# Kernel tuning notes

Measured on AMD Instinct MI355X. Metric: run time of the kernel, lower is better.

The kernel has to match this reference:

```python
import jax, jax.numpy as jnp
import numpy as np

NDIM = 128
GDIM = 128
NUM_LAYERS = 2
B = 8192
IDX = 16          # nodes per graph
EPG = 32          # edges per graph
N = B * IDX       # total nodes = 131072
E = B * EPG       # total edges = 262144


def setup_inputs() -> dict:
    key = jax.random.key(0)
    ks = jax.random.split(key, 24)
    h = jax.random.normal(ks[0], (B, IDX, NDIM), dtype=jnp.float32)
    # edges constrained within each graph (flattened node indexing)
    gid = jnp.repeat(jnp.arange(B, dtype=jnp.int64), EPG)
    src = gid * IDX + jax.random.randint(ks[1], (E,), 0, IDX).astype(jnp.int64)
    dst = gid * IDX + jax.random.randint(ks[2], (E,), 0, IDX).astype(jnp.int64)
    edge_index = jnp.stack([src, dst], axis=0)
    s = 0.05
    inp = {
        'h': h,
        'edge_index': edge_index,
        'msg_W': jax.random.normal(ks[3], (NUM_LAYERS, 2 * NDIM, 2 * NDIM), jnp.float32) * s,
        'msg_b': jax.random.normal(ks[4], (NUM_LAYERS, 2 * NDIM), jnp.float32) * s,
        'msgr_W': jax.random.normal(ks[5], (NUM_LAYERS, 2 * NDIM, 2 * NDIM), jnp.float32) * s,
        'msgr_b': jax.random.normal(ks[6], (NUM_LAYERS, 2 * NDIM), jnp.float32) * s,
        'gru_Wih': jax.random.normal(ks[7], (NUM_LAYERS, 3 * NDIM, 2 * NDIM), jnp.float32) * s,
        'gru_Whh': jax.random.normal(ks[8], (NUM_LAYERS, 3 * NDIM, NDIM), jnp.float32) * s,
        'gru_bih': jax.random.normal(ks[9], (NUM_LAYERS, 3 * NDIM), jnp.float32) * s,
        'gru_bhh': jax.random.normal(ks[10], (NUM_LAYERS, 3 * NDIM), jnp.float32) * s,
        'fm_W': jax.random.normal(ks[11], (GDIM, NDIM), jnp.float32) * s,
        'fm_b': jax.random.normal(ks[12], (GDIM,), jnp.float32) * s,
        'gm_W': jax.random.normal(ks[13], (1, NDIM), jnp.float32) * s,
        'gm_b': jax.random.normal(ks[14], (1,), jnp.float32) * s,
        'fmi_W': jax.random.normal(ks[15], (GDIM, NDIM), jnp.float32) * s,
        'fmi_b': jax.random.normal(ks[16], (GDIM,), jnp.float32) * s,
        'gmi_W': jax.random.normal(ks[17], (1, NDIM), jnp.float32) * s,
        'gmi_b': jax.random.normal(ks[18], (1,), jnp.float32) * s,
    }
    return inp


def _gnn_forward(h, edge_index, msg_W, msg_b, msgr_W, msgr_b,
                 gru_Wih, gru_Whh, gru_bih, gru_bhh):
    # h: [N, ndim]; edge_index: [2, E] -> doubled with reversed edges -> [2, 2E]
    ei = jnp.concatenate([edge_index, edge_index[::-1]], axis=1)
    src, dst = ei[0], ei[1]
    e = edge_index.shape[1]
    n_nodes = h.shape[0]
    for l in range(NUM_LAYERS):
        # (eval mode: dropout p=0.0 is a no-op)
        h_j = h[src]                       # [2E, ndim]
        h_i = h[dst]                       # [2E, ndim]
        m = jnp.concatenate([h_j, h_i], axis=1)   # [2E, 2*ndim]
        m_fwd, m_rev = m[:e], m[e:]
        a = jnp.concatenate([
            m_fwd @ msg_W[l].T + msg_b[l],
            m_rev @ msgr_W[l].T + msgr_b[l],
        ], axis=0)                          # [2E, 2*ndim]
        aggr = jax.ops.segment_sum(a, dst, num_segments=n_nodes)  # [N, 2*ndim]
        # GRUCell(aggr, h): gate order r, z, n (torch convention)
        gi = aggr @ gru_Wih[l].T + gru_bih[l]   # [N, 3*ndim]
        gh = h @ gru_Whh[l].T + gru_bhh[l]      # [N, 3*ndim]
        gi_r, gi_z, gi_n = jnp.split(gi, 3, axis=1)
        gh_r, gh_z, gh_n = jnp.split(gh, 3, axis=1)
        r = jax.nn.sigmoid(gi_r + gh_r)
        z = jax.nn.sigmoid(gi_z + gh_z)
        n = jnp.tanh(gi_n + r * gh_n)
        h = n + z * (h - n)                 # (1-z)*n + z*h
    return h


def _graph_aggr(h, idx, f_W, f_b, g_W, g_b):
    # gated sum aggregation
    h_vG = h @ f_W.T + f_b                      # [N, gdim]
    g_vG = jax.nn.sigmoid(h @ g_W.T + g_b)      # [N, 1]
    out = (h_vG * g_vG).reshape(-1, idx, f_W.shape[0])
    return out.sum(axis=1)                      # [B, gdim]


def reference(h, edge_index, msg_W, msg_b, msgr_W, msgr_b,
              gru_Wih, gru_Whh, gru_bih, gru_bhh,
              fm_W, fm_b, gm_W, gm_b, fmi_W, fmi_b, gmi_W, gmi_b):
    idx = h.shape[1]
    hf = h.reshape(-1, NDIM)
    hf = _gnn_forward(hf, edge_index, msg_W, msg_b, msgr_W, msgr_b,
                      gru_Wih, gru_Whh, gru_bih, gru_bhh)
    h_G = _graph_aggr(hf, idx, fm_W, fm_b, gm_W, gm_b)
    h_G_init = _graph_aggr(hf, idx, fmi_W, fmi_b, gmi_W, gmi_b)
    return (hf.reshape(-1, idx, NDIM), h_G, h_G_init)
```

## Files before the change

### kernel.cpp

```cpp
#include <hip/hip_runtime.h>
#include <math.h>
#include <stdint.h>

#define NDIM 128
#define B_GRAPHS 8192
#define IDX 16
#define EPG 32
#define NN (B_GRAPHS*IDX)
#define NE (B_GRAPHS*EPG)

typedef short bf16x8 __attribute__((ext_vector_type(8)));
typedef float f32x4  __attribute__((ext_vector_type(4)));
typedef unsigned short u16x4 __attribute__((ext_vector_type(4)));

__device__ inline unsigned short f2bf(float x) {
    union { float f; unsigned u; } v; v.f = x;
    unsigned r = v.u + 0x7fff + ((v.u >> 16) & 1);
    return (unsigned short)(r >> 16);
}
__device__ inline float bf2f(unsigned short b) {
    union { unsigned u; float f; } v; v.u = ((unsigned)b) << 16;
    return v.f;
}
__device__ inline float sigm(float x) { return 1.f/(1.f + __expf(-x)); }
__device__ inline float tanh_f(float x) {
    float ax = fabsf(x);
    float t  = __expf(-2.f*ax);
    float r  = (1.f - t)/(1.f + t);
    return copysignf(r, x);
}

#define GLOAD_LDS16(g, l) \
    __builtin_amdgcn_global_load_lds( \
        (const __attribute__((address_space(1))) unsigned int*)(g), \
        (__attribute__((address_space(3))) unsigned int*)(l), 16, 0, 0)

__global__ __launch_bounds__(256) void compose_kernel(
    const float* __restrict__ msg_W, const float* __restrict__ msgr_W,
    const float* __restrict__ Wih,   const float* __restrict__ Whh,
    const float* __restrict__ msg_b, const float* __restrict__ msgr_b,
    unsigned short* __restrict__ WB, float* __restrict__ c34)
{
    int idx = blockIdx.x*256 + threadIdx.x;
    const int TWB = 2*512*640;
    if (idx < TWB) {
        int l = idx / (512*640); int rem = idx - l*(512*640);
        int c = rem / 640; int k = rem - c*640;
        float val;
        if (k < 512) {
            if (c < 384) {
                const float* wih = Wih + l*384*256 + c*256;
                const float* M; int sc;
                if (k < 128)      { M = msg_W  + l*256*256; sc = k;       }
                else if (k < 256) { M = msgr_W + l*256*256; sc = k - 128; }
                else if (k < 384) { M = msg_W  + l*256*256; sc = k - 128; }
                else              { M = msgr_W + l*256*256; sc = k - 256; }
                float acc = 0.f;
                for (int q = 0; q < 256; q++) acc = fmaf(wih[q], M[q*256 + sc], acc);
                val = acc;
            } else val = 0.f;
        } else {
            int kk = k - 512;
            if (c < 256)      val = Whh[l*384*128 + c*128 + kk];
            else if (c < 384) val = 0.f;
            else              val = Whh[l*384*128 + (c-128)*128 + kk];
        }
        WB[idx] = f2bf(val);
    } else if (idx < TWB + 2*2*384) {
        int i2 = idx - TWB;
        int l = i2 / 768; int rem = i2 - l*768;
        int which = rem / 384; int r = rem - which*384;
        const float* wih = Wih + l*384*256 + r*256;
        const float* bb  = (which ? msgr_b : msg_b) + l*256;
        float acc = 0.f;
        for (int q = 0; q < 256; q++) acc = fmaf(wih[q], bb[q], acc);
        c34[l*768 + which*384 + r] = acc;
    }
}

__global__ __launch_bounds__(128) void init_kernel(
    const float* __restrict__ hin, const int* __restrict__ ei,
    unsigned short* __restrict__ A, float* __restrict__ indeg,
    float* __restrict__ outdeg, unsigned char* __restrict__ pack)
{
    int g = blockIdx.x, t = threadIdx.x;
    __shared__ float hb[16][128];
    __shared__ float sin_[16][128];
    __shared__ float sout_[16][128];
    __shared__ int sl[32], dl[32];
    __shared__ int cin[16], cout[16];
    __shared__ int flag64;
    int base = g*IDX;
    for (int r = 0; r < 16; r++) hb[r][t] = hin[(size_t)(base+r)*128 + t];
    for (int r = 0; r < 16; r++) { sin_[r][t] = 0.f; sout_[r][t] = 0.f; }
    if (t < 16) { cin[t] = 0; cout[t] = 0; }
    if (t == 0) {
        int orv = 0;
        for (int i = 1; i < 64; i += 2) orv |= ei[i];
        flag64 = (orv == 0);
    }
    __syncthreads();
    if (t < 32) {
        int e = g*EPG + t;
        int sv, dv;
        if (flag64) { sv = ei[2*e]; dv = ei[2*(NE + e)]; }
        else        { sv = ei[e];   dv = ei[NE + e];     }
        sl[t] = sv - base; dl[t] = dv - base;
        atomicAdd(&cout[sl[t]], 1); atomicAdd(&cin[dl[t]], 1);
        pack[g*32 + t] = (unsigned char)((sl[t] & 15) | ((dl[t] & 15) << 4));
    }
    __syncthreads();
    for (int e = 0; e < 32; e++) {
        sin_[dl[e]][t]  += hb[sl[e]][t];
        sout_[sl[e]][t] += hb[dl[e]][t];
    }
    for (int r = 0; r < 16; r++) {
        size_t v = base + r;
        float di = (float)cin[r], dof = (float)cout[r];
        A[v*640 + t]        = f2bf(sin_[r][t]);
        A[v*640 + 128 + t]  = f2bf(sout_[r][t]);
        A[v*640 + 256 + t]  = f2bf(di  * hb[r][t]);
        A[v*640 + 384 + t]  = f2bf(dof * hb[r][t]);
        A[v*640 + 512 + t]  = f2bf(hb[r][t]);
    }
    if (t < 16) { indeg[base+t] = (float)cin[t]; outdeg[base+t] = (float)cout[t]; }
}

struct LoopBufs { unsigned short As[3][4096]; unsigned short Bs[3][16384]; };
union UnionRegion {
    LoopBufs lp;
    unsigned short Gs[512*128];
    float sio[2][128][128];
};
struct SmemT { UnionRegion u; unsigned short hnewB[128][128]; };

__device__ __forceinline__ void stage_tile(
    const unsigned short* __restrict__ A, const unsigned short* __restrict__ WB,
    int n0, int kc, unsigned short* As, unsigned short* Bs, int tid)
{
    {
        int row = tid >> 2, s = tid & 3;
        int slot = s ^ ((row >> 2) & 3);
        GLOAD_LDS16(A + (size_t)(n0 + row)*640 + kc + slot*8, As + row*32 + s*8);
    }
#pragma unroll
    for (int i = 0; i < 4; i++) {
        int u = i*512 + tid; int col = u >> 2, s = u & 3;
        int slot = s ^ ((col >> 2) & 3);
        GLOAD_LDS16(WB + (size_t)col*640 + kc + slot*8, Bs + col*32 + s*8);
    }
}

template <bool FINAL>
__global__ __launch_bounds__(512, 2) void fused_kernel(
    unsigned short* __restrict__ A,
    const unsigned short* __restrict__ WB,
    const float* __restrict__ indeg, const float* __restrict__ outdeg,
    const unsigned char* __restrict__ pack,
    const float* __restrict__ c34l,
    const float* __restrict__ bihl, const float* __restrict__ bhhl,
    float* __restrict__ hf)
{
    __shared__ SmemT sm;
    const int n0  = blockIdx.x * 128;
    const int tid = threadIdx.x;
    const int lane = tid & 63;
    const int wc  = tid >> 6;
    const int l15 = lane & 15, l4 = lane >> 4;

    int ks_lo = 0, ks_hi = 20;
    if (wc == 4 || wc == 5) ks_hi = 16;
    if (wc >= 6)            ks_lo = 16;

    f32x4 acc[8][4] = {};

    stage_tile(A, WB, n0, 0,  sm.u.lp.As[0], sm.u.lp.Bs[0], tid);
    stage_tile(A, WB, n0, 32, sm.u.lp.As[1], sm.u.lp.Bs[1], tid);
    asm volatile("s_waitcnt vmcnt(5)\n\ts_barrier" ::: "memory");

    for (int ks = 0; ks < 20; ks++) {
        int buf = ks % 3;
        if (ks + 2 < 20) {
            int nb = (ks + 2) % 3;
            stage_tile(A, WB, n0, (ks+2)*32, sm.u.lp.As[nb], sm.u.lp.Bs[nb], tid);
        }
        if (ks >= ks_lo && ks < ks_hi) {
            bf16x8 af[8], bfv[4];
            int slot = l4 ^ ((l15 >> 2) & 3);
            const unsigned short* Asb = sm.u.lp.As[buf];
            const unsigned short* Bsb = sm.u.lp.Bs[buf];
#pragma unroll
            for (int mi = 0; mi < 8; mi++)
                af[mi] = *(const bf16x8*)(Asb + (mi*16 + l15)*32 + slot*8);
#pragma unroll
            for (int ni = 0; ni < 4; ni++)
                bfv[ni] = *(const bf16x8*)(Bsb + (wc*64 + ni*16 + l15)*32 + slot*8);
#pragma unroll
            for (int mi = 0; mi < 8; mi++)
#pragma unroll
                for (int ni = 0; ni < 4; ni++)
                    acc[mi][ni] = __builtin_amdgcn_mfma_f32_16x16x32_bf16(
                        af[mi], bfv[ni], acc[mi][ni], 0, 0, 0);
        }
        if (ks + 2 < 20)
            asm volatile("s_waitcnt vmcnt(5)\n\ts_barrier" ::: "memory");
        else
            asm volatile("s_waitcnt vmcnt(0)\n\ts_barrier" ::: "memory");
    }

#pragma unroll
    for (int mi = 0; mi < 8; mi++) {
        int row0  = mi*16 + l4*4;
        int slotA = row0 >> 3;
        int half  = (row0 >> 2) & 1;
#pragma unroll
        for (int ni = 0; ni < 4; ni++) {
            int col = wc*64 + ni*16 + l15;
            int slot2 = slotA ^ (col & 15);
            u16x4 w;
            w[0] = f2bf(acc[mi][ni][0]); w[1] = f2bf(acc[mi][ni][1]);
            w[2] = f2bf(acc[mi][ni][2]); w[3] = f2bf(acc[mi][ni][3]);
            *(u16x4*)((char*)sm.u.Gs + col*256 + slot2*16 + half*8) = w;
        }
    }
    __syncthreads();

    const int c = tid & 127;
    const int q = tid >> 7;
    float c3r = c34l[c],     c3z = c34l[128+c], c3n = c34l[256+c];
    float c4r = c34l[384+c], c4z = c34l[512+c], c4n = c34l[640+c];
    float br   = bihl[c]     + bhhl[c];
    float bz   = bihl[128+c] + bhhl[128+c];
    float bin_ = bihl[256+c];
    float bhn  = bhhl[256+c];

    float hnew[2][16];
#pragma unroll
    for (int i = 0; i < 2; i++) {
        int gl = q*2 + i, r0 = gl*16;
#pragma unroll
        for (int rg = 0; rg < 4; rg++) {
            int row0 = r0 + rg*4;
            u16x4 sv[4];
#pragma unroll
            for (int seg = 0; seg < 4; seg++) {
                int col = seg*128 + c;
                int slot2 = (row0 >> 3) ^ (col & 15);
                sv[seg] = *(const u16x4*)((const char*)sm.u.Gs
                            + col*256 + slot2*16 + ((row0 >> 2) & 1)*8);
            }
#pragma unroll
            for (int j = 0; j < 4; j++) {
                int row = row0 + j; size_t v = (size_t)n0 + row;
                float di = indeg[v], dof = outdeg[v];
                float Gr  = bf2f(sv[0][j]), Gz  = bf2f(sv[1][j]);
                float Gin = bf2f(sv[2][j]), Ghn = bf2f(sv[3][j]);
                float hold = bf2f(A[v*640 + 512 + c]);
                float rr = sigm(Gr + di*c3r + dof*c4r + br);
                float zz = sigm(Gz + di*c3z + dof*c4z + bz);
                float nn = tanh_f(Gin + di*c3n + dof*c4n + bin_ + rr*(Ghn + bhn));
                float hv = nn + zz*(hold - nn);
                if (FINAL) hf[v*128 + c] = hv;
                else { hnew[i][rg*4 + j] = hv; sm.hnewB[row][c] = f2bf(hv); }
            }
        }
    }

    if (!FINAL) {
        __syncthreads();
#pragma unroll
        for (int i = 0; i < 2; i++) {
            int gl = q*2 + i, r0 = gl*16;
#pragma unroll
            for (int d = 0; d < 16; d++) {
                sm.u.sio[0][r0 + d][c] = 0.f;
                sm.u.sio[1][r0 + d][c] = 0.f;
            }
            size_t g = (size_t)(n0 >> 4) + gl;
            const unsigned int* pk = (const unsigned int*)(pack + g*32);
#pragma unroll
            for (int j = 0; j < 8; j++) {
                unsigned int u4 = pk[j];
#pragma unroll
                for (int b = 0; b < 4; b++) {
                    int p = (u4 >> (b*8)) & 255;
                    int s = p & 15, d = p >> 4;
                    sm.u.sio[0][r0 + d][c] += bf2f(sm.hnewB[r0 + s][c]);
                    sm.u.sio[1][r0 + s][c] += bf2f(sm.hnewB[r0 + d][c]);
                }
            }
#pragma unroll
            for (int d = 0; d < 16; d++) {
                int row = r0 + d; size_t v = (size_t)n0 + row;
                float di = indeg[v], dof = outdeg[v];
                float hv = hnew[i][d];
                A[v*640 + c]       = f2bf(sm.u.sio[0][row][c]);
                A[v*640 + 128 + c] = f2bf(sm.u.sio[1][row][c]);
                A[v*640 + 256 + c] = f2bf(di  * hv);
                A[v*640 + 384 + c] = f2bf(dof * hv);
                A[v*640 + 512 + c] = f2bf(hv);
            }
        }
    }
}

__global__ __launch_bounds__(256) void pool_kernel(
    const float* __restrict__ hf,
    const float* __restrict__ gm_W,  const float* __restrict__ gm_b,
    const float* __restrict__ gmi_W, const float* __restrict__ gmi_b,
    float* __restrict__ P1, float* __restrict__ P2, float* __restrict__ sg)
{
    const int t = threadIdx.x;
    const int nbase = blockIdx.x * 256;
    __shared__ float g1s[256], g2s[256];

    {
        const float4* hp = (const float4*)(hf + (size_t)(nbase + t)*128);
        float a1 = 0.f, a2 = 0.f;
#pragma unroll
        for (int k = 0; k < 32; k++) {
            float4 hv = hp[k];
            float4 w1 = ((const float4*)gm_W)[k];
            float4 w2 = ((const float4*)gmi_W)[k];
            a1 = fmaf(hv.x,w1.x,fmaf(hv.y,w1.y,fmaf(hv.z,w1.z,fmaf(hv.w,w1.w,a1))));
            a2 = fmaf(hv.x,w2.x,fmaf(hv.y,w2.y,fmaf(hv.z,w2.z,fmaf(hv.w,w2.w,a2))));
        }
        g1s[t] = sigm(a1 + gm_b[0]);
        g2s[t] = sigm(a2 + gmi_b[0]);
    }
    __syncthreads();

    int c  = t & 127;
    int gh = t >> 7;
#pragma unroll
    for (int i = 0; i < 8; i++) {
        int glc = gh*8 + i;
        float p1 = 0.f, p2 = 0.f;
#pragma unroll
        for (int r = 0; r < 16; r++) {
            float x = hf[(size_t)(nbase + glc*16 + r)*128 + c];
            p1 = fmaf(g1s[glc*16+r], x, p1);
            p2 = fmaf(g2s[glc*16+r], x, p2);
        }
        size_t g = nbase/16 + glc;
        P1[g*128 + c] = p1;
        P2[g*128 + c] = p2;
    }
    if (t < 32) {
        int glc = t >> 1, which = t & 1;
        const float* gs = which ? g2s : g1s;
        float s = 0.f;
        for (int r = 0; r < 16; r++) s += gs[glc*16+r];
        sg[(nbase/16 + glc)*2 + which] = s;
    }
}

__global__ __launch_bounds__(256) void outgemm_kernel(
    const float* __restrict__ P1, const float* __restrict__ P2,
    const float* __restrict__ sg,
    const float* __restrict__ fm_W,  const float* __restrict__ fm_b,
    const float* __restrict__ fmi_W, const float* __restrict__ fmi_b,
    float* __restrict__ out1, float* __restrict__ out2)
{
    const int g0 = blockIdx.x * 32;
    const int t  = threadIdx.x;
    __shared__ float Ws[128][33];
    __shared__ float Ps[32][33];
    const int tc = t & 15, tg = t >> 4;

    for (int pass = 0; pass < 2; pass++) {
        const float* P  = pass ? P2 : P1;
        const float* W  = pass ? fmi_W : fm_W;
        const float* bb = pass ? fmi_b : fm_b;
        float acc[2][8] = {};
        for (int kc = 0; kc < 128; kc += 32) {
#pragma unroll
            for (int i = 0; i < 16; i++) {
                int u = i*256 + t; int r = u >> 5, k = u & 31;
                Ws[r][k] = W[(size_t)r*128 + kc + k];
            }
#pragma unroll
            for (int i = 0; i < 4; i++) {
                int u = i*256 + t; int r = u >> 5, k = u & 31;
                Ps[r][k] = P[(size_t)(g0 + r)*128 + kc + k];
            }
            __syncthreads();
#pragma unroll 8
            for (int k = 0; k < 32; k++) {
                float p0 = Ps[tg*2][k], p1v = Ps[tg*2+1][k];
#pragma unroll
                for (int j = 0; j < 8; j++) {
                    float w = Ws[tc*8+j][k];
                    acc[0][j] = fmaf(p0,  w, acc[0][j]);
                    acc[1][j] = fmaf(p1v, w, acc[1][j]);
                }
            }
            __syncthreads();
        }
        float* outp = pass ? out2 : out1;
#pragma unroll
        for (int i = 0; i < 2; i++) {
            int g = g0 + tg*2 + i;
            float sgv = sg[g*2 + pass];
#pragma unroll
            for (int j = 0; j < 8; j++) {
                int cc = tc*8 + j;
                outp[(size_t)g*128 + cc] = acc[i][j] + bb[cc]*sgv;
            }
        }
    }
}

extern "C" void kernel_launch(void* const* d_in, const int* in_sizes, int n_in,
                              void* d_out, int out_size, void* d_ws, size_t ws_size,
                              hipStream_t stream)
{
    const float* h     = (const float*)d_in[0];
    const int*   ei    = (const int*)d_in[1];
    const float* msgW  = (const float*)d_in[2];
    const float* msgb  = (const float*)d_in[3];
    const float* msgrW = (const float*)d_in[4];
    const float* msgrb = (const float*)d_in[5];
    const float* Wih   = (const float*)d_in[6];
    const float* Whh   = (const float*)d_in[7];
    const float* bih   = (const float*)d_in[8];
    const float* bhh   = (const float*)d_in[9];
    const float* fmW   = (const float*)d_in[10];
    const float* fmb   = (const float*)d_in[11];
    const float* gmW   = (const float*)d_in[12];
    const float* gmb   = (const float*)d_in[13];
    const float* fmiW  = (const float*)d_in[14];
    const float* fmib  = (const float*)d_in[15];
    const float* gmiW  = (const float*)d_in[16];
    const float* gmib  = (const float*)d_in[17];

    char* w = (char*)d_ws;
    unsigned short* A    = (unsigned short*)w;  w += (size_t)NN*640*2;
    unsigned short* WB   = (unsigned short*)w;  w += (size_t)2*512*640*2;
    float* c34   = (float*)w;                   w += (size_t)2*768*4;
    float* indeg = (float*)w;                   w += (size_t)NN*4;
    float* outdeg= (float*)w;                   w += (size_t)NN*4;
    unsigned char* pack = (unsigned char*)w;    w += (size_t)B_GRAPHS*32;
    float* P1    = (float*)w;                   w += (size_t)B_GRAPHS*128*4;
    float* P2    = (float*)w;                   w += (size_t)B_GRAPHS*128*4;
    float* sgb   = (float*)w;                   w += (size_t)B_GRAPHS*2*4;

    float* hf   = (float*)d_out;
    float* out1 = hf + (size_t)NN*128;
    float* out2 = out1 + (size_t)B_GRAPHS*128;

    int compose_items = 2*512*640 + 2*2*384;
    compose_kernel<<<(compose_items + 255)/256, 256, 0, stream>>>(
        msgW, msgrW, Wih, Whh, msgb, msgrb, WB, c34);

    init_kernel<<<B_GRAPHS, 128, 0, stream>>>(h, ei, A, indeg, outdeg, pack);

    fused_kernel<false><<<NN/128, 512, 0, stream>>>(
        A, WB, indeg, outdeg, pack, c34, bih, bhh, nullptr);
    fused_kernel<true><<<NN/128, 512, 0, stream>>>(
        A, WB + (size_t)512*640, indeg, outdeg, pack,
        c34 + 768, bih + 384, bhh + 384, hf);

    pool_kernel<<<NN/256, 256, 0, stream>>>(
        hf, gmW, gmb, gmiW, gmib, P1, P2, sgb);
    outgemm_kernel<<<B_GRAPHS/32, 256, 0, stream>>>(
        P1, P2, sgb, fmW, fmb, fmiW, fmib, out1, out2);
}
```

Measured before the change: 451.0 us.

## Fuse init, both GNN layers and pooling into one persistent-tile mega kernel

Replaces the init kernel, the two fused layer kernels and the pool kernel with a single kernel that keeps each 128-node tile's hidden state and aggregated messages in LDS across both layers. Edge aggregation uses a per-graph CSR built in shared memory, and the degree-scaled operands are formed on the fly from LDS. Weights are read directly from global memory in a permuted column order instead of being staged through LDS. This drops the large bf16 A buffer round-trips through global memory and several launches. In exchange the weight fragments are no longer staged through LDS, and pooling now reads bf16 hidden state rather than fp32, which can change accuracy slightly.

```diff
diff --git a/kernel.cpp b/kernel.cpp
--- a/kernel.cpp
+++ b/kernel.cpp
@@ -11,7 +11,6 @@
 
 typedef short bf16x8 __attribute__((ext_vector_type(8)));
 typedef float f32x4  __attribute__((ext_vector_type(4)));
-typedef unsigned short u16x4 __attribute__((ext_vector_type(4)));
 
 __device__ inline unsigned short f2bf(float x) {
     union { float f; unsigned u; } v; v.f = x;
@@ -29,11 +28,6 @@
     float r  = (1.f - t)/(1.f + t);
     return copysignf(r, x);
 }
-
-#define GLOAD_LDS16(g, l) \
-    __builtin_amdgcn_global_load_lds( \
-        (const __attribute__((address_space(1))) unsigned int*)(g), \
-        (__attribute__((address_space(3))) unsigned int*)(l), 16, 0, 0)
 
 __global__ __launch_bounds__(256) void compose_kernel(
     const float* __restrict__ msg_W, const float* __restrict__ msgr_W,
@@ -45,11 +39,11 @@
     const int TWB = 2*512*640;
     if (idx < TWB) {
         int l = idx / (512*640); int rem = idx - l*(512*640);
-        int c = rem / 640; int k = rem - c*640;
+        int cold = rem / 640; int k = rem - cold*640;
         float val;
         if (k < 512) {
-            if (c < 384) {
-                const float* wih = Wih + l*384*256 + c*256;
+            if (cold < 384) {
+                const float* wih = Wih + l*384*256 + cold*256;
                 const float* M; int sc;
                 if (k < 128)      { M = msg_W  + l*256*256; sc = k;       }
                 else if (k < 256) { M = msgr_W + l*256*256; sc = k - 128; }
@@ -61,11 +55,13 @@
             } else val = 0.f;
         } else {
             int kk = k - 512;
-            if (c < 256)      val = Whh[l*384*128 + c*128 + kk];
-            else if (c < 384) val = 0.f;
-            else              val = Whh[l*384*128 + (c-128)*128 + kk];
-        }
-        WB[idx] = f2bf(val);
+            if (cold < 256)      val = Whh[l*384*128 + cold*128 + kk];
+            else if (cold < 384) val = 0.f;
+            else                 val = Whh[l*384*128 + (cold-128)*128 + kk];
+        }
+        int cc = cold & 127, t = cold >> 7;
+        int colp = ((cc >> 5) << 7) + (t << 5) + (cc & 31);
+        WB[l*512*640 + colp*640 + k] = f2bf(val);
     } else if (idx < TWB + 2*2*384) {
         int i2 = idx - TWB;
         int l = i2 / 768; int rem = i2 - l*768;
@@ -78,280 +74,300 @@
     }
 }
 
-__global__ __launch_bounds__(128) void init_kernel(
+struct MegaSmem {
+    unsigned short S[128*256];
+    unsigned short hreg[128*128];
+    unsigned char sl8[256], dl8[256];
+    unsigned char csr[8][2][17];
+    unsigned char adj[8][2][32];
+    unsigned char off[8][2][16];
+    float degf[128][2];
+    float gates[2][128];
+    int flag64;
+};
+
+__device__ __forceinline__ int s_addr(int row, int e) {
+    return row*512 + (((e>>3) ^ (row&7))<<4) + ((e&7)<<1);
+}
+__device__ __forceinline__ int h_addr(int row, int c) {
+    return row*256 + (((c>>3) ^ (row&7))<<4) + ((c&7)<<1);
+}
+
+__device__ __forceinline__ void gatherS(MegaSmem& sm, int tid) {
+    int c = tid & 127, gq = tid >> 7;
+    for (int gi2 = 0; gi2 < 2; gi2++) {
+        int gl = gq + gi2*4, rb = gl*16;
+        for (int d = 0; d < 16; d++) {
+            float a = 0.f;
+            int s0 = sm.csr[gl][0][d], s1 = sm.csr[gl][0][d+1];
+            for (int j = s0; j < s1; j++)
+                a += bf2f(*(const unsigned short*)((const char*)sm.hreg
+                        + h_addr(rb + sm.adj[gl][0][j], c)));
+            *(unsigned short*)((char*)sm.S + s_addr(rb + d, c)) = f2bf(a);
+            float b = 0.f;
+            s0 = sm.csr[gl][1][d]; s1 = sm.csr[gl][1][d+1];
+            for (int j = s0; j < s1; j++)
+                b += bf2f(*(const unsigned short*)((const char*)sm.hreg
+                        + h_addr(rb + sm.adj[gl][1][j], c)));
+            *(unsigned short*)((char*)sm.S + s_addr(rb + d, 128 + c)) = f2bf(b);
+        }
+    }
+}
+
+#define MF(a,b,c) __builtin_amdgcn_mfma_f32_16x16x32_bf16((a),(b),(c),0,0,0)
+#define LB(t,cct,kt) (*(const bf16x8*)(WBl + (size_t)(ch*128 + (t)*32 + (cct)*16 + l15)*640 + (kt)*32 + l4*8))
+
+__global__ __launch_bounds__(512, 2) void mega_kernel(
     const float* __restrict__ hin, const int* __restrict__ ei,
-    unsigned short* __restrict__ A, float* __restrict__ indeg,
-    float* __restrict__ outdeg, unsigned char* __restrict__ pack)
+    const unsigned short* __restrict__ WB, const float* __restrict__ c34,
+    const float* __restrict__ bih, const float* __restrict__ bhh,
+    const float* __restrict__ gmW,  const float* __restrict__ gmb,
+    const float* __restrict__ gmiW, const float* __restrict__ gmib,
+    float* __restrict__ hf, float* __restrict__ P1, float* __restrict__ P2,
+    float* __restrict__ sg)
 {
-    int g = blockIdx.x, t = threadIdx.x;
-    __shared__ float hb[16][128];
-    __shared__ float sin_[16][128];
-    __shared__ float sout_[16][128];
-    __shared__ int sl[32], dl[32];
-    __shared__ int cin[16], cout[16];
-    __shared__ int flag64;
-    int base = g*IDX;
-    for (int r = 0; r < 16; r++) hb[r][t] = hin[(size_t)(base+r)*128 + t];
-    for (int r = 0; r < 16; r++) { sin_[r][t] = 0.f; sout_[r][t] = 0.f; }
-    if (t < 16) { cin[t] = 0; cout[t] = 0; }
-    if (t == 0) {
+    __shared__ MegaSmem sm;
+    const int n0  = blockIdx.x * 128;
+    const int g0  = blockIdx.x * 8;
+    const int tid = threadIdx.x;
+    const int lane = tid & 63, wid = tid >> 6;
+    const int rh = wid >> 2, ch = wid & 3;
+    const int l15 = lane & 15, l4 = lane >> 4;
+    const int rowb = rh * 64;
+
+    if (tid == 0) {
         int orv = 0;
         for (int i = 1; i < 64; i += 2) orv |= ei[i];
-        flag64 = (orv == 0);
-    }
-    __syncthreads();
-    if (t < 32) {
-        int e = g*EPG + t;
+        sm.flag64 = (orv == 0);
+    }
+    for (int i = 0; i < 32; i++) {
+        int idx = i*512 + tid; int row = idx >> 7, c = idx & 127;
+        float v = hin[(size_t)(n0 + row)*128 + c];
+        *(unsigned short*)((char*)sm.hreg + h_addr(row, c)) = f2bf(v);
+    }
+    __syncthreads();
+    if (tid < 256) {
+        int gl = tid >> 5;
+        int e = (g0 + gl)*32 + (tid & 31);
         int sv, dv;
-        if (flag64) { sv = ei[2*e]; dv = ei[2*(NE + e)]; }
-        else        { sv = ei[e];   dv = ei[NE + e];     }
-        sl[t] = sv - base; dl[t] = dv - base;
-        atomicAdd(&cout[sl[t]], 1); atomicAdd(&cin[dl[t]], 1);
-        pack[g*32 + t] = (unsigned char)((sl[t] & 15) | ((dl[t] & 15) << 4));
-    }
-    __syncthreads();
-    for (int e = 0; e < 32; e++) {
-        sin_[dl[e]][t]  += hb[sl[e]][t];
-        sout_[sl[e]][t] += hb[dl[e]][t];
-    }
-    for (int r = 0; r < 16; r++) {
-        size_t v = base + r;
-        float di = (float)cin[r], dof = (float)cout[r];
-        A[v*640 + t]        = f2bf(sin_[r][t]);
-        A[v*640 + 128 + t]  = f2bf(sout_[r][t]);
-        A[v*640 + 256 + t]  = f2bf(di  * hb[r][t]);
-        A[v*640 + 384 + t]  = f2bf(dof * hb[r][t]);
-        A[v*640 + 512 + t]  = f2bf(hb[r][t]);
-    }
-    if (t < 16) { indeg[base+t] = (float)cin[t]; outdeg[base+t] = (float)cout[t]; }
-}
-
-struct LoopBufs { unsigned short As[3][4096]; unsigned short Bs[3][16384]; };
-union UnionRegion {
-    LoopBufs lp;
-    unsigned short Gs[512*128];
-    float sio[2][128][128];
-};
-struct SmemT { UnionRegion u; unsigned short hnewB[128][128]; };
-
-__device__ __forceinline__ void stage_tile(
-    const unsigned short* __restrict__ A, const unsigned short* __restrict__ WB,
-    int n0, int kc, unsigned short* As, unsigned short* Bs, int tid)
-{
+        if (sm.flag64) { sv = ei[2*e]; dv = ei[2*(NE + e)]; }
+        else           { sv = ei[e];   dv = ei[NE + e];     }
+        sm.sl8[tid] = (unsigned char)(sv - (g0 + gl)*16);
+        sm.dl8[tid] = (unsigned char)(dv - (g0 + gl)*16);
+    }
+    __syncthreads();
+    if (tid < 16) {
+        int gl = tid >> 1, dir = tid & 1;
+        const unsigned char* key = dir ? sm.sl8 : sm.dl8;
+        const unsigned char* val = dir ? sm.dl8 : sm.sl8;
+        unsigned char* C = sm.csr[gl][dir];
+        for (int d = 0; d < 17; d++) C[d] = 0;
+        for (int e2 = 0; e2 < 32; e2++) C[key[gl*32 + e2] + 1]++;
+        for (int d = 0; d < 16; d++) { C[d+1] += C[d]; sm.off[gl][dir][d] = C[d]; }
+        for (int e2 = 0; e2 < 32; e2++) {
+            int k = key[gl*32 + e2];
+            sm.adj[gl][dir][sm.off[gl][dir][k]++] = val[gl*32 + e2];
+        }
+    }
+    __syncthreads();
+    if (tid < 128) {
+        int gl = tid >> 4, d = tid & 15;
+        sm.degf[tid][0] = (float)(sm.csr[gl][0][d+1] - sm.csr[gl][0][d]);
+        sm.degf[tid][1] = (float)(sm.csr[gl][1][d+1] - sm.csr[gl][1][d]);
+    }
+    __syncthreads();
+    gatherS(sm, tid);
+    __syncthreads();
+
+    for (int l = 0; l < 2; l++) {
+        const unsigned short* WBl = WB + (size_t)l*512*640;
+        const float* c34l = c34 + l*768;
+        const float* bihl = bih + l*384;
+        const float* bhhl = bhh + l*384;
+
+        float dia[4], doa[4];
+#pragma unroll
+        for (int mi = 0; mi < 4; mi++) {
+            int row = rowb + mi*16 + l15;
+            dia[mi] = sm.degf[row][0];
+            doa[mi] = sm.degf[row][1];
+        }
+
+        f32x4 acc[4][8] = {};
+
+#pragma unroll
+        for (int kt = 0; kt < 8; kt++) {
+            bf16x8 b0 = LB(0,0,kt), b1 = LB(0,1,kt), b2 = LB(1,0,kt),
+                   b3 = LB(1,1,kt), b4 = LB(2,0,kt), b5 = LB(2,1,kt);
+            bf16x8 a_[4];
+#pragma unroll
+            for (int mi = 0; mi < 4; mi++) {
+                int row = rowb + mi*16 + l15;
+                int phys = (kt*4 + l4) ^ (row & 7);
+                a_[mi] = *(const bf16x8*)((const char*)sm.S + row*512 + phys*16);
+            }
+#pragma unroll
+            for (int mi = 0; mi < 4; mi++) {
+                acc[mi][0]=MF(a_[mi],b0,acc[mi][0]); acc[mi][1]=MF(a_[mi],b1,acc[mi][1]);
+                acc[mi][2]=MF(a_[mi],b2,acc[mi][2]); acc[mi][3]=MF(a_[mi],b3,acc[mi][3]);
+                acc[mi][4]=MF(a_[mi],b4,acc[mi][4]); acc[mi][5]=MF(a_[mi],b5,acc[mi][5]);
+            }
+        }
+#pragma unroll
+        for (int kt = 8; kt < 12; kt++) {
+            bf16x8 b0 = LB(0,0,kt), b1 = LB(0,1,kt), b2 = LB(1,0,kt),
+                   b3 = LB(1,1,kt), b4 = LB(2,0,kt), b5 = LB(2,1,kt);
+            bf16x8 a_[4];
+#pragma unroll
+            for (int mi = 0; mi < 4; mi++) {
+                int row = rowb + mi*16 + l15;
+                int phys = ((kt-8)*4 + l4) ^ (row & 7);
+                bf16x8 hv = *(const bf16x8*)((const char*)sm.hreg + row*256 + phys*16);
+                float s = dia[mi];
+#pragma unroll
+                for (int j = 0; j < 8; j++)
+                    a_[mi][j] = (short)f2bf(bf2f((unsigned short)hv[j]) * s);
+            }
+#pragma unroll
+            for (int mi = 0; mi < 4; mi++) {
+                acc[mi][0]=MF(a_[mi],b0,acc[mi][0]); acc[mi][1]=MF(a_[mi],b1,acc[mi][1]);
+                acc[mi][2]=MF(a_[mi],b2,acc[mi][2]); acc[mi][3]=MF(a_[mi],b3,acc[mi][3]);
+                acc[mi][4]=MF(a_[mi],b4,acc[mi][4]); acc[mi][5]=MF(a_[mi],b5,acc[mi][5]);
+            }
+        }
+#pragma unroll
+        for (int kt = 12; kt < 16; kt++) {
+            bf16x8 b0 = LB(0,0,kt), b1 = LB(0,1,kt), b2 = LB(1,0,kt),
+                   b3 = LB(1,1,kt), b4 = LB(2,0,kt), b5 = LB(2,1,kt);
+            bf16x8 a_[4];
+#pragma unroll
+            for (int mi = 0; mi < 4; mi++) {
+                int row = rowb + mi*16 + l15;
+                int phys = ((kt-12)*4 + l4) ^ (row & 7);
+                bf16x8 hv = *(const bf16x8*)((const char*)sm.hreg + row*256 + phys*16);
+                float s = doa[mi];
+#pragma unroll
+                for (int j = 0; j < 8; j++)
+                    a_[mi][j] = (short)f2bf(bf2f((unsigned short)hv[j]) * s);
+            }
+#pragma unroll
+            for (int mi = 0; mi < 4; mi++) {
+                acc[mi][0]=MF(a_[mi],b0,acc[mi][0]); acc[mi][1]=MF(a_[mi],b1,acc[mi][1]);
+                acc[mi][2]=MF(a_[mi],b2,acc[mi][2]); acc[mi][3]=MF(a_[mi],b3,acc[mi][3]);
+                acc[mi][4]=MF(a_[mi],b4,acc[mi][4]); acc[mi][5]=MF(a_[mi],b5,acc[mi][5]);
+            }
+        }
+#pragma unroll
+        for (int kt = 16; kt < 20; kt++) {
+            bf16x8 b0 = LB(0,0,kt), b1 = LB(0,1,kt), b2 = LB(1,0,kt),
+                   b3 = LB(1,1,kt), b4 = LB(3,0,kt), b5 = LB(3,1,kt);
+            bf16x8 a_[4];
+#pragma unroll
+            for (int mi = 0; mi < 4; mi++) {
+                int row = rowb + mi*16 + l15;
+                int phys = ((kt-16)*4 + l4) ^ (row & 7);
+                a_[mi] = *(const bf16x8*)((const char*)sm.hreg + row*256 + phys*16);
+            }
+#pragma unroll
+            for (int mi = 0; mi < 4; mi++) {
+                acc[mi][0]=MF(a_[mi],b0,acc[mi][0]); acc[mi][1]=MF(a_[mi],b1,acc[mi][1]);
+                acc[mi][2]=MF(a_[mi],b2,acc[mi][2]); acc[mi][3]=MF(a_[mi],b3,acc[mi][3]);
+                acc[mi][6]=MF(a_[mi],b4,acc[mi][6]); acc[mi][7]=MF(a_[mi],b5,acc[mi][7]);
+            }
+        }
+
+        f32x4 hn[4][2];
+#pragma unroll
+        for (int cct = 0; cct < 2; cct++) {
+            int c = ch*32 + cct*16 + l15;
+            float c3r = c34l[c],     c3z = c34l[128+c], c3n = c34l[256+c];
+            float c4r = c34l[384+c], c4z = c34l[512+c], c4n = c34l[640+c];
+            float br   = bihl[c]     + bhhl[c];
+            float bz   = bihl[128+c] + bhhl[128+c];
+            float bin_ = bihl[256+c];
+            float bhn_ = bhhl[256+c];
+#pragma unroll
+            for (int mi = 0; mi < 4; mi++) {
+                f32x4 R = acc[mi][cct], Z = acc[mi][2+cct];
+                f32x4 GI = acc[mi][4+cct], GH = acc[mi][6+cct];
+                f32x4 out;
+#pragma unroll
+                for (int q = 0; q < 4; q++) {
+                    int row = rowb + mi*16 + l4*4 + q;
+                    float di = sm.degf[row][0], dof = sm.degf[row][1];
+                    float hold = bf2f(*(const unsigned short*)((const char*)sm.hreg
+                                      + h_addr(row, c)));
+                    float rr = sigm(R[q]  + di*c3r + dof*c4r + br);
+                    float zz = sigm(Z[q]  + di*c3z + dof*c4z + bz);
+                    float nn = tanh_f(GI[q] + di*c3n + dof*c4n + bin_
+                                      + rr*(GH[q] + bhn_));
+                    out[q] = nn + zz*(hold - nn);
+                }
+                hn[mi][cct] = out;
+            }
+        }
+        __syncthreads();
+#pragma unroll
+        for (int cct = 0; cct < 2; cct++) {
+            int c = ch*32 + cct*16 + l15;
+#pragma unroll
+            for (int mi = 0; mi < 4; mi++) {
+#pragma unroll
+                for (int q = 0; q < 4; q++) {
+                    int row = rowb + mi*16 + l4*4 + q;
+                    *(unsigned short*)((char*)sm.hreg + h_addr(row, c))
+                        = f2bf(hn[mi][cct][q]);
+                    if (l == 1)
+                        hf[(size_t)(n0 + row)*128 + c] = hn[mi][cct][q];
+                }
+            }
+        }
+        __syncthreads();
+        if (l == 0) {
+            gatherS(sm, tid);
+            __syncthreads();
+        }
+    }
+
+    if (tid < 128) {
+        int row = tid;
+        float a1 = 0.f, a2 = 0.f;
+        for (int s = 0; s < 16; s++) {
+            int phys = s ^ (row & 7);
+            bf16x8 hv = *(const bf16x8*)((const char*)sm.hreg + row*256 + phys*16);
+#pragma unroll
+            for (int j = 0; j < 8; j++) {
+                float x = bf2f((unsigned short)hv[j]);
+                int c = s*8 + j;
+                a1 = fmaf(gmW[c],  x, a1);
+                a2 = fmaf(gmiW[c], x, a2);
+            }
+        }
+        sm.gates[0][row] = sigm(a1 + gmb[0]);
+        sm.gates[1][row] = sigm(a2 + gmib[0]);
+    }
+    __syncthreads();
     {
-        int row = tid >> 2, s = tid & 3;
-        int slot = s ^ ((row >> 2) & 3);
-        GLOAD_LDS16(A + (size_t)(n0 + row)*640 + kc + slot*8, As + row*32 + s*8);
-    }
-#pragma unroll
-    for (int i = 0; i < 4; i++) {
-        int u = i*512 + tid; int col = u >> 2, s = u & 3;
-        int slot = s ^ ((col >> 2) & 3);
-        GLOAD_LDS16(WB + (size_t)col*640 + kc + slot*8, Bs + col*32 + s*8);
-    }
-}
-
-template <bool FINAL>
-__global__ __launch_bounds__(512, 2) void fused_kernel(
-    unsigned short* __restrict__ A,
-    const unsigned short* __restrict__ WB,
-    const float* __restrict__ indeg, const float* __restrict__ outdeg,
-    const unsigned char* __restrict__ pack,
-    const float* __restrict__ c34l,
-    const float* __restrict__ bihl, const float* __restrict__ bhhl,
-    float* __restrict__ hf)
-{
-    __shared__ SmemT sm;
-    const int n0  = blockIdx.x * 128;
-    const int tid = threadIdx.x;
-    const int lane = tid & 63;
-    const int wc  = tid >> 6;
-    const int l15 = lane & 15, l4 = lane >> 4;
-
-    int ks_lo = 0, ks_hi = 20;
-    if (wc == 4 || wc == 5) ks_hi = 16;
-    if (wc >= 6)            ks_lo = 16;
-
-    f32x4 acc[8][4] = {};
-
-    stage_tile(A, WB, n0, 0,  sm.u.lp.As[0], sm.u.lp.Bs[0], tid);
-    stage_tile(A, WB, n0, 32, sm.u.lp.As[1], sm.u.lp.Bs[1], tid);
-    asm volatile("s_waitcnt vmcnt(5)\n\ts_barrier" ::: "memory");
-
-    for (int ks = 0; ks < 20; ks++) {
-        int buf = ks % 3;
-        if (ks + 2 < 20) {
-            int nb = (ks + 2) % 3;
-            stage_tile(A, WB, n0, (ks+2)*32, sm.u.lp.As[nb], sm.u.lp.Bs[nb], tid);
-        }
-        if (ks >= ks_lo && ks < ks_hi) {
-            bf16x8 af[8], bfv[4];
-            int slot = l4 ^ ((l15 >> 2) & 3);
-            const unsigned short* Asb = sm.u.lp.As[buf];
-            const unsigned short* Bsb = sm.u.lp.Bs[buf];
-#pragma unroll
-            for (int mi = 0; mi < 8; mi++)
-                af[mi] = *(const bf16x8*)(Asb + (mi*16 + l15)*32 + slot*8);
-#pragma unroll
-            for (int ni = 0; ni < 4; ni++)
-                bfv[ni] = *(const bf16x8*)(Bsb + (wc*64 + ni*16 + l15)*32 + slot*8);
-#pragma unroll
-            for (int mi = 0; mi < 8; mi++)
-#pragma unroll
-                for (int ni = 0; ni < 4; ni++)
-                    acc[mi][ni] = __builtin_amdgcn_mfma_f32_16x16x32_bf16(
-                        af[mi], bfv[ni], acc[mi][ni], 0, 0, 0);
-        }
-        if (ks + 2 < 20)
-            asm volatile("s_waitcnt vmcnt(5)\n\ts_barrier" ::: "memory");
-        else
-            asm volatile("s_waitcnt vmcnt(0)\n\ts_barrier" ::: "memory");
-    }
-
-#pragma unroll
-    for (int mi = 0; mi < 8; mi++) {
-        int row0  = mi*16 + l4*4;
-        int slotA = row0 >> 3;
-        int half  = (row0 >> 2) & 1;
-#pragma unroll
-        for (int ni = 0; ni < 4; ni++) {
-            int col = wc*64 + ni*16 + l15;
-            int slot2 = slotA ^ (col & 15);
-            u16x4 w;
-            w[0] = f2bf(acc[mi][ni][0]); w[1] = f2bf(acc[mi][ni][1]);
-            w[2] = f2bf(acc[mi][ni][2]); w[3] = f2bf(acc[mi][ni][3]);
-            *(u16x4*)((char*)sm.u.Gs + col*256 + slot2*16 + half*8) = w;
-        }
-    }
-    __syncthreads();
-
-    const int c = tid & 127;
-    const int q = tid >> 7;
-    float c3r = c34l[c],     c3z = c34l[128+c], c3n = c34l[256+c];
-    float c4r = c34l[384+c], c4z = c34l[512+c], c4n = c34l[640+c];
-    float br   = bihl[c]     + bhhl[c];
-    float bz   = bihl[128+c] + bhhl[128+c];
-    float bin_ = bihl[256+c];
-    float bhn  = bhhl[256+c];
-
-    float hnew[2][16];
-#pragma unroll
-    for (int i = 0; i < 2; i++) {
-        int gl = q*2 + i, r0 = gl*16;
-#pragma unroll
-        for (int rg = 0; rg < 4; rg++) {
-            int row0 = r0 + rg*4;
-            u16x4 sv[4];
-#pragma unroll
-            for (int seg = 0; seg < 4; seg++) {
-                int col = seg*128 + c;
-                int slot2 = (row0 >> 3) ^ (col & 15);
-                sv[seg] = *(const u16x4*)((const char*)sm.u.Gs
-                            + col*256 + slot2*16 + ((row0 >> 2) & 1)*8);
-            }
-#pragma unroll
-            for (int j = 0; j < 4; j++) {
-                int row = row0 + j; size_t v = (size_t)n0 + row;
-                float di = indeg[v], dof = outdeg[v];
-                float Gr  = bf2f(sv[0][j]), Gz  = bf2f(sv[1][j]);
-                float Gin = bf2f(sv[2][j]), Ghn = bf2f(sv[3][j]);
-                float hold = bf2f(A[v*640 + 512 + c]);
-                float rr = sigm(Gr + di*c3r + dof*c4r + br);
-                float zz = sigm(Gz + di*c3z + dof*c4z + bz);
-                float nn = tanh_f(Gin + di*c3n + dof*c4n + bin_ + rr*(Ghn + bhn));
-                float hv = nn + zz*(hold - nn);
-                if (FINAL) hf[v*128 + c] = hv;
-                else { hnew[i][rg*4 + j] = hv; sm.hnewB[row][c] = f2bf(hv); }
-            }
-        }
-    }
-
-    if (!FINAL) {
-        __syncthreads();
-#pragma unroll
-        for (int i = 0; i < 2; i++) {
-            int gl = q*2 + i, r0 = gl*16;
-#pragma unroll
-            for (int d = 0; d < 16; d++) {
-                sm.u.sio[0][r0 + d][c] = 0.f;
-                sm.u.sio[1][r0 + d][c] = 0.f;
-            }
-            size_t g = (size_t)(n0 >> 4) + gl;
-            const unsigned int* pk = (const unsigned int*)(pack + g*32);
-#pragma unroll
-            for (int j = 0; j < 8; j++) {
-                unsigned int u4 = pk[j];
-#pragma unroll
-                for (int b = 0; b < 4; b++) {
-                    int p = (u4 >> (b*8)) & 255;
-                    int s = p & 15, d = p >> 4;
-                    sm.u.sio[0][r0 + d][c] += bf2f(sm.hnewB[r0 + s][c]);
-                    sm.u.sio[1][r0 + s][c] += bf2f(sm.hnewB[r0 + d][c]);
-                }
-            }
-#pragma unroll
-            for (int d = 0; d < 16; d++) {
-                int row = r0 + d; size_t v = (size_t)n0 + row;
-                float di = indeg[v], dof = outdeg[v];
-                float hv = hnew[i][d];
-                A[v*640 + c]       = f2bf(sm.u.sio[0][row][c]);
-                A[v*640 + 128 + c] = f2bf(sm.u.sio[1][row][c]);
-                A[v*640 + 256 + c] = f2bf(di  * hv);
-                A[v*640 + 384 + c] = f2bf(dof * hv);
-                A[v*640 + 512 + c] = f2bf(hv);
-            }
-        }
-    }
-}
-
-__global__ __launch_bounds__(256) void pool_kernel(
-    const float* __restrict__ hf,
-    const float* __restrict__ gm_W,  const float* __restrict__ gm_b,
-    const float* __restrict__ gmi_W, const float* __restrict__ gmi_b,
-    float* __restrict__ P1, float* __restrict__ P2, float* __restrict__ sg)
-{
-    const int t = threadIdx.x;
-    const int nbase = blockIdx.x * 256;
-    __shared__ float g1s[256], g2s[256];
-
-    {
-        const float4* hp = (const float4*)(hf + (size_t)(nbase + t)*128);
-        float a1 = 0.f, a2 = 0.f;
-#pragma unroll
-        for (int k = 0; k < 32; k++) {
-            float4 hv = hp[k];
-            float4 w1 = ((const float4*)gm_W)[k];
-            float4 w2 = ((const float4*)gmi_W)[k];
-            a1 = fmaf(hv.x,w1.x,fmaf(hv.y,w1.y,fmaf(hv.z,w1.z,fmaf(hv.w,w1.w,a1))));
-            a2 = fmaf(hv.x,w2.x,fmaf(hv.y,w2.y,fmaf(hv.z,w2.z,fmaf(hv.w,w2.w,a2))));
-        }
-        g1s[t] = sigm(a1 + gm_b[0]);
-        g2s[t] = sigm(a2 + gmi_b[0]);
-    }
-    __syncthreads();
-
-    int c  = t & 127;
-    int gh = t >> 7;
-#pragma unroll
-    for (int i = 0; i < 8; i++) {
-        int glc = gh*8 + i;
-        float p1 = 0.f, p2 = 0.f;
-#pragma unroll
-        for (int r = 0; r < 16; r++) {
-            float x = hf[(size_t)(nbase + glc*16 + r)*128 + c];
-            p1 = fmaf(g1s[glc*16+r], x, p1);
-            p2 = fmaf(g2s[glc*16+r], x, p2);
-        }
-        size_t g = nbase/16 + glc;
-        P1[g*128 + c] = p1;
-        P2[g*128 + c] = p2;
-    }
-    if (t < 32) {
-        int glc = t >> 1, which = t & 1;
-        const float* gs = which ? g2s : g1s;
+        int c = tid & 127, gq = tid >> 7;
+        for (int gi2 = 0; gi2 < 2; gi2++) {
+            int gl = gq + gi2*4, rb = gl*16;
+            float p1 = 0.f, p2 = 0.f;
+            for (int r = 0; r < 16; r++) {
+                float x = bf2f(*(const unsigned short*)((const char*)sm.hreg
+                               + h_addr(rb + r, c)));
+                p1 = fmaf(sm.gates[0][rb + r], x, p1);
+                p2 = fmaf(sm.gates[1][rb + r], x, p2);
+            }
+            size_t g = g0 + gl;
+            P1[g*128 + c] = p1;
+            P2[g*128 + c] = p2;
+        }
+    }
+    if (tid < 16) {
+        int gl = tid >> 1, w = tid & 1;
         float s = 0.f;
-        for (int r = 0; r < 16; r++) s += gs[glc*16+r];
-        sg[(nbase/16 + glc)*2 + which] = s;
+        for (int r = 0; r < 16; r++) s += sm.gates[w][gl*16 + r];
+        sg[(size_t)(g0 + gl)*2 + w] = s;
     }
 }
 
@@ -435,15 +451,11 @@
     const float* gmib  = (const float*)d_in[17];
 
     char* w = (char*)d_ws;
-    unsigned short* A    = (unsigned short*)w;  w += (size_t)NN*640*2;
-    unsigned short* WB   = (unsigned short*)w;  w += (size_t)2*512*640*2;
-    float* c34   = (float*)w;                   w += (size_t)2*768*4;
-    float* indeg = (float*)w;                   w += (size_t)NN*4;
-    float* outdeg= (float*)w;                   w += (size_t)NN*4;
-    unsigned char* pack = (unsigned char*)w;    w += (size_t)B_GRAPHS*32;
-    float* P1    = (float*)w;                   w += (size_t)B_GRAPHS*128*4;
-    float* P2    = (float*)w;                   w += (size_t)B_GRAPHS*128*4;
-    float* sgb   = (float*)w;                   w += (size_t)B_GRAPHS*2*4;
+    unsigned short* WB = (unsigned short*)w;  w += (size_t)2*512*640*2;
+    float* c34   = (float*)w;                 w += (size_t)2*768*4;
+    float* P1    = (float*)w;                 w += (size_t)B_GRAPHS*128*4;
+    float* P2    = (float*)w;                 w += (size_t)B_GRAPHS*128*4;
+    float* sgb   = (float*)w;                 w += (size_t)B_GRAPHS*2*4;
 
     float* hf   = (float*)d_out;
     float* out1 = hf + (size_t)NN*128;
@@ -453,16 +465,9 @@
     compose_kernel<<<(compose_items + 255)/256, 256, 0, stream>>>(
         msgW, msgrW, Wih, Whh, msgb, msgrb, WB, c34);
 
-    init_kernel<<<B_GRAPHS, 128, 0, stream>>>(h, ei, A, indeg, outdeg, pack);
-
-    fused_kernel<false><<<NN/128, 512, 0, stream>>>(
-        A, WB, indeg, outdeg, pack, c34, bih, bhh, nullptr);
-    fused_kernel<true><<<NN/128, 512, 0, stream>>>(
-        A, WB + (size_t)512*640, indeg, outdeg, pack,
-        c34 + 768, bih + 384, bhh + 384, hf);
-
-    pool_kernel<<<NN/256, 256, 0, stream>>>(
-        hf, gmW, gmb, gmiW, gmib, P1, P2, sgb);
+    mega_kernel<<<NN/128, 512, 0, stream>>>(
+        h, ei, WB, c34, bih, bhh, gmW, gmb, gmiW, gmib, hf, P1, P2, sgb);
+
     outgemm_kernel<<<B_GRAPHS/32, 256, 0, stream>>>(
         P1, P2, sgb, fmW, fmb, fmiW, fmib, out1, out2);
 }
```

Result: slower. 774.2 us (+71.7%).
